# Kernel tuning notes

Hardware: AMD Instinct MI355X
Metric: run time of the kernel (lower is better)

Reference implementation:

```python
import jax, jax.numpy as jnp
import numpy as np
import math

B, L, D, H = 2, 2048, 1024, 16
DH = D // H  # 64


def setup_inputs() -> dict:
    key = jax.random.key(0)
    ks = jax.random.split(key, 8)
    s = 1.0 / math.sqrt(D)
    return {
        "query": jax.random.normal(ks[0], (B, L, D), dtype=jnp.float32),
        "key": jax.random.normal(ks[1], (B, L, D), dtype=jnp.float32),
        "value": jax.random.normal(ks[2], (B, L, D), dtype=jnp.float32),
        "attn_mask": jax.random.bernoulli(ks[3], 0.1, (B, L, L)),  # True = masked
        "Wq": jax.random.normal(ks[4], (D, D), dtype=jnp.float32) * s,
        "Wk": jax.random.normal(ks[5], (D, D), dtype=jnp.float32) * s,
        "Wv": jax.random.normal(ks[6], (D, D), dtype=jnp.float32) * s,
        "Wo": jax.random.normal(ks[7], (D, D), dtype=jnp.float32) * s,
    }


def reference(query, key, value, attn_mask, Wq, Wk, Wv, Wo):
    # torch nn.Linear computes x @ W.T (bias=False here)
    def shape(x):
        b, l, _ = x.shape
        return x.reshape(b, l, H, DH).transpose(0, 2, 1, 3)  # [B,H,L,DH]

    q = shape(query @ Wq.T) / jnp.sqrt(jnp.float32(DH))
    k = shape(key @ Wk.T)
    v = shape(value @ Wv.T)

    scores = jnp.einsum("bhqd,bhkd->bhqk", q, k)  # [B,H,Q,K]
    if attn_mask is not None:
        scores = jnp.where(attn_mask[:, None, :, :], jnp.float32(-1e18), scores)
    attn = jax.nn.softmax(scores, axis=-1)
    # dropout p=0.0 (eval/deterministic) -> identity
    context = jnp.einsum("bhqk,bhkd->bhqd", attn, v)
    context = context.transpose(0, 2, 1, 3).reshape(query.shape[0], -1, D)
    output = context @ Wo.T
    top_attn = attn[:, 0, :, :]
    return output, top_attn
```

## Files before the change

kernel.cpp:

```cpp
#include <hip/hip_runtime.h>

#define BB 2
#define LL 2048
#define DD 1024
#define HH 16
#define DHH 64

typedef _Float16 f16;
typedef _Float16 f16x8 __attribute__((ext_vector_type(8)));
typedef _Float16 f16x4 __attribute__((ext_vector_type(4)));
typedef _Float16 f16x2 __attribute__((ext_vector_type(2)));
typedef float f32x4 __attribute__((ext_vector_type(4)));
typedef unsigned long long u64;

#define VWAIT(N) asm volatile("s_waitcnt vmcnt(" #N ")" ::: "memory")
#define SB0() __builtin_amdgcn_sched_barrier(0)

__device__ __forceinline__ void gload_lds16(const void* g, void* l) {
    __builtin_amdgcn_global_load_lds(
        (const __attribute__((address_space(1))) void*)g,
        (__attribute__((address_space(3))) void*)l, 16, 0, 0);
}

__device__ __forceinline__ f16x4 cvt4f(float4 v) {
    f16x4 o;
    o[0] = (f16)v.x; o[1] = (f16)v.y; o[2] = (f16)v.z; o[3] = (f16)v.w;
    return o;
}

__global__ void prep(const float* __restrict__ q, const float* __restrict__ k,
                     const float* __restrict__ v, const int* __restrict__ msk,
                     const float* __restrict__ wq, const float* __restrict__ wk,
                     const float* __restrict__ wv, const float* __restrict__ wo,
                     f16* __restrict__ bufQ, f16* __restrict__ bufK, f16* __restrict__ bufV,
                     f16* __restrict__ wh, u64* __restrict__ Mp, float scq) {
    const int tid = threadIdx.x;
    const int y = blockIdx.y;
    if (y == 0) {
        const int lane = tid & 63;
        int w = (blockIdx.x * 256 + tid) >> 6;
        const int nw = (1024 * 256) >> 6;
        for (; w < BB * LL * 32; w += nw) {
            int mv = msk[(size_t)w * 64 + lane];
            u64 bits = __ballot(mv != 0);
            if (lane == 0) {
                const int kt = w & 31;
                const int bq = w >> 5;
                const int qq = bq & 2047, b = bq >> 11;
                Mp[((size_t)b * 32 + kt) * LL + qq] = bits;
            }
        }
    } else if (y == 1) {
        int i = blockIdx.x * 256 + tid;
        const int stride = 1024 * 256;
        for (; i < 4 * 262144; i += stride) {
            const int sel = i >> 18, j = i & 262143;
            const float* s = sel == 0 ? wq : sel == 1 ? wk : sel == 2 ? wv : wo;
            ((f16x4*)wh)[i] = cvt4f(((const float4*)s)[j]);
        }
    } else {
        const float* s = y == 2 ? q : y == 3 ? k : v;
        f16* o = y == 2 ? bufQ : y == 3 ? bufK : bufV;
        const float sc = y == 2 ? scq : 1.0f;
        int i = blockIdx.x * 256 + tid;
        const int stride = 1024 * 256;
        for (; i < (int)(BB * LL * DD / 4); i += stride) {
            float4 vv = ((const float4*)s)[i];
            vv.x *= sc; vv.y *= sc; vv.z *= sc; vv.w *= sc;
            ((f16x4*)o)[i] = cvt4f(vv);
        }
    }
}

__global__ void cvt_kernel(const float* __restrict__ src, f16* __restrict__ dst, int n4, float sc) {
    int i = blockIdx.x * blockDim.x + threadIdx.x;
    const int stride = gridDim.x * blockDim.x;
    for (; i < n4; i += stride) {
        float4 v = ((const float4*)src)[i];
        v.x *= sc; v.y *= sc; v.z *= sc; v.w *= sc;
        ((f16x4*)dst)[i] = cvt4f(v);
    }
}
__global__ void cvt4_kernel(const float* __restrict__ a, const float* __restrict__ b,
                            const float* __restrict__ c, const float* __restrict__ d,
                            f16* __restrict__ dst, int n4) {
    const float* s = blockIdx.y == 0 ? a : blockIdx.y == 1 ? b : blockIdx.y == 2 ? c : d;
    f16* o = dst + (size_t)blockIdx.y * n4 * 4;
    int i = blockIdx.x * blockDim.x + threadIdx.x;
    const int stride = gridDim.x * blockDim.x;
    for (; i < n4; i += stride)
        ((f16x4*)o)[i] = cvt4f(((const float4*)s)[i]);
}
__global__ void pack_mask(const int* __restrict__ mask, u64* __restrict__ out, int nwords) {
    const int lane = threadIdx.x & 63;
    int w = (blockIdx.x * blockDim.x + threadIdx.x) >> 6;
    const int nw = (gridDim.x * blockDim.x) >> 6;
    for (; w < nwords; w += nw) {
        int mv = mask[(size_t)w * 64 + lane];
        u64 bits = __ballot(mv != 0);
        if (lane == 0) {
            const int kt = w & 31;
            const int bq = w >> 5;
            const int qq = bq & 2047, b = bq >> 11;
            out[((size_t)b * 32 + kt) * LL + qq] = bits;
        }
    }
}

__device__ __forceinline__ void gemm_core(const f16* __restrict__ A, const f16* __restrict__ W,
                                          f16* __restrict__ C, int z, int xb, int yb, char* lds) {
    const int tid = threadIdx.x, wid = tid >> 6, lane = tid & 63;
    const int m0 = yb * 128, n0 = xb * 128;
    const int lq = lane & 15, lg = lane >> 4;
    const int wm = (wid >> 1) << 6, wn = (wid & 1) << 6;
    f32x4 acc[4][4] = {};

    #pragma unroll
    for (int t = 0; t < 2; ++t)
        #pragma unroll
        for (int j = 0; j < 2; ++j) {
            const int ldsoff = (wid * 2 + j) << 10;
            const int o = ldsoff + lane * 16;
            const int row = o >> 6, c8 = (o >> 4) & 3;
            gload_lds16(A + (size_t)(m0 + row) * DD + t * 32 + c8 * 8, lds + t * 8192 + ldsoff);
            gload_lds16(W + (size_t)(n0 + row) * DD + t * 32 + c8 * 8, lds + 24576 + t * 8192 + ldsoff);
        }

    for (int kt = 0; kt < 32; ++kt) {
        VWAIT(4);
        SB0();
        __builtin_amdgcn_s_barrier();
        SB0();
        {
            const int nk = (kt + 2 < 32) ? kt + 2 : 31;
            const int nb = (kt + 2) % 3;
            #pragma unroll
            for (int j = 0; j < 2; ++j) {
                const int ldsoff = (wid * 2 + j) << 10;
                const int o = ldsoff + lane * 16;
                const int row = o >> 6, c8 = (o >> 4) & 3;
                gload_lds16(A + (size_t)(m0 + row) * DD + nk * 32 + c8 * 8,
                            lds + nb * 8192 + ldsoff);
                gload_lds16(W + (size_t)(n0 + row) * DD + nk * 32 + c8 * 8,
                            lds + 24576 + nb * 8192 + ldsoff);
            }
        }
        SB0();

        const int cb = kt % 3;
        const char* Ab = lds + cb * 8192;
        const char* Bb = lds + 24576 + cb * 8192;
        f16x8 af[4], bf[4];
        #pragma unroll
        for (int m = 0; m < 4; ++m)
            af[m] = *(const f16x8*)(Ab + (wm + m * 16 + lq) * 64 + lg * 16);
        #pragma unroll
        for (int n = 0; n < 4; ++n)
            bf[n] = *(const f16x8*)(Bb + (wn + n * 16 + lq) * 64 + lg * 16);
        __builtin_amdgcn_s_setprio(1);
        #pragma unroll
        for (int m = 0; m < 4; ++m)
            #pragma unroll
            for (int n = 0; n < 4; ++n)
                acc[m][n] = __builtin_amdgcn_mfma_f32_16x16x32_f16(af[m], bf[n], acc[m][n], 0, 0, 0);
        __builtin_amdgcn_s_setprio(0);
    }

    #pragma unroll
    for (int m = 0; m < 4; ++m)
        #pragma unroll
        for (int n = 0; n < 4; ++n)
            #pragma unroll
            for (int r = 0; r < 4; ++r) {
                const int row = m0 + wm + m * 16 + lg * 4 + r;
                const int col = n0 + wn + n * 16 + lq;
                const float val = acc[m][n][r];
                if (z < 2) {
                    C[(size_t)row * DD + col] = (f16)val;
                } else {
                    const int b = row >> 11, l = row & 2047;
                    const int h = col >> 6, dh = col & 63;
                    C[((size_t)((b * HH + h) * DHH + dh) << 11) + l] = (f16)val;
                }
            }
}

__global__ __launch_bounds__(256) void gemm_qkv(
        const f16* __restrict__ A0, const f16* __restrict__ A1, const f16* __restrict__ A2,
        const f16* __restrict__ W0, const f16* __restrict__ W1, const f16* __restrict__ W2,
        f16* __restrict__ C0, f16* __restrict__ C1, f16* __restrict__ C2) {
    __shared__ __align__(16) char lds[49152];
    const int bid = blockIdx.x;
    const int xcd = bid & 7, j = bid >> 3;
    const int p = xcd * 12 + (j >> 3);
    const int xb = j & 7;
    const int z = p >> 5, yb = p & 31;
    const f16* A = z == 0 ? A0 : z == 1 ? A1 : A2;
    const f16* W = z == 0 ? W0 : z == 1 ? W1 : W2;
    f16* C       = z == 0 ? C0 : z == 1 ? C1 : C2;
    gemm_core(A, W, C, z, xb, yb, lds);
}

__global__ __launch_bounds__(256) void gemm_one(const f16* __restrict__ A, const f16* __restrict__ W,
                                                f16* __restrict__ C, int z) {
    __shared__ __align__(16) char lds[49152];
    gemm_core(A, W, C, z, blockIdx.x, blockIdx.y, lds);
}

template<bool TOPF16>
__global__ __launch_bounds__(256) void finale(const f16* __restrict__ A, const f16* __restrict__ W,
                                              float* __restrict__ C, float* __restrict__ top,
                                              const void* __restrict__ src,
                                              const float* __restrict__ linvp) {
    __shared__ __align__(16) char lds[36864];
    const int tid = threadIdx.x;
    if (blockIdx.x >= 512) {
        int i = (blockIdx.x - 512) * 256 + tid;
        const int stride = 1024 * 256;
        if (TOPF16) {
            const f16x8* s8 = (const f16x8*)src;
            const int n = (int)((size_t)BB * LL * LL / 8);
            for (; i < n; i += stride) {
                f16x8 v = s8[i];
                const float linv = linvp[(i * 8) >> 11];
                float4 a, bq;
                a.x = (float)v[0] * linv; a.y = (float)v[1] * linv;
                a.z = (float)v[2] * linv; a.w = (float)v[3] * linv;
                bq.x = (float)v[4] * linv; bq.y = (float)v[5] * linv;
                bq.z = (float)v[6] * linv; bq.w = (float)v[7] * linv;
                ((float4*)top)[i * 2] = a;
                ((float4*)top)[i * 2 + 1] = bq;
            }
        } else {
            const int n = (int)((size_t)BB * LL * LL / 4);
            for (; i < n; i += stride) {
                float4 v = ((const float4*)top)[i];
                const float linv = linvp[(i * 4) >> 11];
                v.x = __builtin_amdgcn_exp2f(v.x) * linv;
                v.y = __builtin_amdgcn_exp2f(v.y) * linv;
                v.z = __builtin_amdgcn_exp2f(v.z) * linv;
                v.w = __builtin_amdgcn_exp2f(v.w) * linv;
                ((float4*)top)[i] = v;
            }
        }
        return;
    }
    const int bid = blockIdx.x;
    const int xcd = bid & 7, j = bid >> 3;
    const int yb = xcd * 4 + (j >> 4);
    const int xb = j & 15;
    const int wid = tid >> 6, lane = tid & 63;
    const int m0 = yb * 128, n0 = xb * 64;
    const int lq = lane & 15, lg = lane >> 4;
    const int wm = wid * 32;
    f32x4 acc[2][4] = {};

    #pragma unroll
    for (int t = 0; t < 2; ++t) {
        #pragma unroll
        for (int j2 = 0; j2 < 2; ++j2) {
            const int o = (j2 * 256 + tid) * 16;
            const int row = o >> 6, c8 = (o >> 4) & 3;
            gload_lds16(A + (size_t)(m0 + row) * DD + t * 32 + c8 * 8,
                        lds + t * 8192 + j2 * 4096 + (wid << 10));
        }
        {
            const int o = tid * 16;
            const int row = o >> 6, c8 = (o >> 4) & 3;
            gload_lds16(W + (size_t)(n0 + row) * DD + t * 32 + c8 * 8,
                        lds + 24576 + t * 4096 + (wid << 10));
        }
    }

    for (int kt = 0; kt < 32; ++kt) {
        VWAIT(3);
        SB0();
        __builtin_amdgcn_s_barrier();
        SB0();
        {
            const int nk = (kt + 2 < 32) ? kt + 2 : 31;
            const int nb = (kt + 2) % 3;
            #pragma unroll
            for (int j2 = 0; j2 < 2; ++j2) {
                const int o = (j2 * 256 + tid) * 16;
                const int row = o >> 6, c8 = (o >> 4) & 3;
                gload_lds16(A + (size_t)(m0 + row) * DD + nk * 32 + c8 * 8,
                            lds + nb * 8192 + j2 * 4096 + (wid << 10));
            }
            {
                const int o = tid * 16;
                const int row = o >> 6, c8 = (o >> 4) & 3;
                gload_lds16(W + (size_t)(n0 + row) * DD + nk * 32 + c8 * 8,
                            lds + 24576 + nb * 4096 + (wid << 10));
            }
        }
        SB0();

        const int cb = kt % 3;
        const char* Ab = lds + cb * 8192;
        const char* Bb = lds + 24576 + cb * 4096;
        f16x8 af[2], bf[4];
        #pragma unroll
        for (int m = 0; m < 2; ++m)
            af[m] = *(const f16x8*)(Ab + (wm + m * 16 + lq) * 64 + lg * 16);
        #pragma unroll
        for (int n = 0; n < 4; ++n)
            bf[n] = *(const f16x8*)(Bb + (n * 16 + lq) * 64 + lg * 16);
        __builtin_amdgcn_s_setprio(1);
        #pragma unroll
        for (int m = 0; m < 2; ++m)
            #pragma unroll
            for (int n = 0; n < 4; ++n)
                acc[m][n] = __builtin_amdgcn_mfma_f32_16x16x32_f16(af[m], bf[n], acc[m][n], 0, 0, 0);
        __builtin_amdgcn_s_setprio(0);
    }

    #pragma unroll
    for (int m = 0; m < 2; ++m)
        #pragma unroll
        for (int n = 0; n < 4; ++n)
            #pragma unroll
            for (int r = 0; r < 4; ++r) {
                const int row = m0 + wm + m * 16 + lg * 4 + r;
                const int col = n0 + n * 16 + lq;
                C[(size_t)row * DD + col] = acc[m][n][r];
            }
}

template<bool TOPF16>
__global__ __launch_bounds__(512) void attn_fwd(const f16* __restrict__ Qp, const f16* __restrict__ Kp,
                                                const f16* __restrict__ VTp,
                                                const u64* __restrict__ Mp,
                                                f16* __restrict__ Op, void* __restrict__ topout,
                                                float* __restrict__ statsLinv) {
    extern __shared__ char lds[];
    const int tid = threadIdx.x, wid = tid >> 6, lane = tid & 63;
    const int lq = lane & 15, lg = lane >> 4;
    const int bid = blockIdx.x;
    const int xcd = bid & 7, j = bid >> 3;
    const int bh = xcd * 4 + (j >> 4);
    const int qt = j & 15;
    const int b = bh >> 4, h = bh & 15;
    const bool topblk = (h == 0);
    const int qrow = qt * 128 + wid * 16 + lq;

    const int srow = tid >> 3;
    const int ssc = ((tid & 7) ^ (srow & 7));
    const f16* ksrc = Kp + (size_t)(b * LL + srow) * DD + h * 64 + ssc * 8;
    const f16* vsrc = VTp + (size_t)((b * HH + h) * DHH + srow) * LL + ssc * 8;
    char* kdst = lds + 16384 + (wid << 10);
    char* vdst = lds + 49152 + (wid << 10);

    f16x8 qf[2];
    #pragma unroll
    for (int kk = 0; kk < 2; ++kk)
        qf[kk] = *(const f16x8*)(Qp + (size_t)(b * LL + qrow) * DD + h * 64 + (kk * 4 + lg) * 8);

    #pragma unroll
    for (int t = 0; t < 2; ++t) {
        gload_lds16(ksrc + (size_t)t * 64 * DD, kdst + t * 8192);
        gload_lds16(vsrc + t * 64, vdst + t * 8192);
    }

    float lsum = 0.f;
    f32x4 acc[4] = {};

    for (int it = 0; it < 16; ++it) {
        const int kt0 = it * 2;
        if (topblk && it > 0) { VWAIT(8); } else { VWAIT(0); }
        SB0();
        __builtin_amdgcn_s_barrier();
        SB0();
        const u64 cm0 = Mp[((size_t)b * 32 + kt0) * LL + qrow];
        const u64 cm1 = Mp[((size_t)b * 32 + kt0 + 1) * LL + qrow];
        SB0();
        #pragma unroll
        for (int t = 0; t < 2; ++t) {
            const int nk = (kt0 + 2 + t < 32) ? kt0 + 2 + t : 31;
            const int nb = (kt0 + 2 + t) & 3;
            gload_lds16(ksrc + (size_t)nk * 64 * DD, kdst + nb * 8192);
            gload_lds16(vsrc + nk * 64, vdst + nb * 8192);
        }
        SB0();

        #pragma unroll
        for (int t = 0; t < 2; ++t) {
            const int cb = (kt0 + t) & 3;
            const char* Kb = lds + 16384 + cb * 8192;
            const char* Vb = lds + 49152 + cb * 8192;
            const u64 cm = t == 0 ? cm0 : cm1;

            f32x4 s[4] = {};
            __builtin_amdgcn_s_setprio(1);
            #pragma unroll
            for (int f = 0; f < 4; ++f)
                #pragma unroll
                for (int kk = 0; kk < 2; ++kk) {
                    const int co = (((kk * 4 + lg) ^ (lq & 7)) << 4);
                    f16x8 kf = *(const f16x8*)(Kb + (f * 16 + lq) * 128 + co);
                    s[f] = __builtin_amdgcn_mfma_f32_16x16x32_f16(kf, qf[kk], s[f], 0, 0, 0);
                }
            __builtin_amdgcn_s_setprio(0);

            const u64 wsh = cm >> (lg * 4);
            const unsigned lo = (unsigned)wsh, hi = (unsigned)(wsh >> 32);
            f16x4 ph[4];
            #pragma unroll
            for (int f = 0; f < 4; ++f) {
                const unsigned nib = ((f < 2) ? (lo >> (f * 16)) : (hi >> ((f - 2) * 16))) & 0xFu;
                #pragma unroll
                for (int r = 0; r < 4; ++r)
                    if (nib & (1u << r)) s[f][r] = -1e18f;
                const float p0 = __builtin_amdgcn_exp2f(s[f][0]);
                const float p1 = __builtin_amdgcn_exp2f(s[f][1]);
                const float p2 = __builtin_amdgcn_exp2f(s[f][2]);
                const float p3 = __builtin_amdgcn_exp2f(s[f][3]);
                lsum += (p0 + p1) + (p2 + p3);
                f16x2 pa = __builtin_bit_cast(f16x2, __builtin_amdgcn_cvt_pkrtz(p0, p1));
                f16x2 pb = __builtin_bit_cast(f16x2, __builtin_amdgcn_cvt_pkrtz(p2, p3));
                ph[f][0] = pa[0]; ph[f][1] = pa[1]; ph[f][2] = pb[0]; ph[f][3] = pb[1];
            }

            if (topblk) {
                if (TOPF16) {
                    f16* T = (f16*)topout;
                    #pragma unroll
                    for (int f = 0; f < 4; ++f)
                        *(f16x4*)(T + ((size_t)b * LL + qrow) * LL + (kt0 + t) * 64 + f * 16 + lg * 4) = ph[f];
                } else {
                    float* T = (float*)topout;
                    #pragma unroll
                    for (int f = 0; f < 4; ++f)
                        *(f32x4*)(T + ((size_t)b * LL + qrow) * LL + (kt0 + t) * 64 + f * 16 + lg * 4) = s[f];
                }
            }

            #pragma unroll
            for (int f = 0; f < 4; ++f) {
                const int chunk = f * 2 + (lg >> 1);
                const int bo = ((chunk ^ (lq & 7)) << 4) + (lg & 1) * 8;
                *(f16x4*)(lds + (wid << 11) + lq * 128 + bo) = ph[f];
            }

            __builtin_amdgcn_s_setprio(1);
            #pragma unroll
            for (int kk = 0; kk < 2; ++kk) {
                const int co = (((kk * 4 + lg) ^ (lq & 7)) << 4);
                f16x8 pf = *(const f16x8*)(lds + (wid << 11) + lq * 128 + co);
                #pragma unroll
                for (int f = 0; f < 4; ++f) {
                    f16x8 vf = *(const f16x8*)(Vb + (f * 16 + lq) * 128 + co);
                    acc[f] = __builtin_amdgcn_mfma_f32_16x16x32_f16(vf, pf, acc[f], 0, 0, 0);
                }
            }
            __builtin_amdgcn_s_setprio(0);
        }
    }

    lsum += __shfl_xor(lsum, 16);
    lsum += __shfl_xor(lsum, 32);
    const float linv = 1.f / lsum;
    #pragma unroll
    for (int f = 0; f < 4; ++f) {
        f16x4 ov;
        #pragma unroll
        for (int r = 0; r < 4; ++r) ov[r] = (f16)(acc[f][r] * linv);
        *(f16x4*)(Op + (size_t)(b * LL + qrow) * DD + h * 64 + f * 16 + lg * 4) = ov;
    }
    if (topblk && lg == 0) statsLinv[(size_t)b * LL + qrow] = linv;
}

extern "C" void kernel_launch(void* const* d_in, const int* in_sizes, int n_in,
                              void* d_out, int out_size, void* d_ws, size_t ws_size,
                              hipStream_t stream) {
    const float* q   = (const float*)d_in[0];
    const float* k   = (const float*)d_in[1];
    const float* v   = (const float*)d_in[2];
    const int*   msk = (const int*)d_in[3];
    const float* wq  = (const float*)d_in[4];
    const float* wk  = (const float*)d_in[5];
    const float* wv  = (const float*)d_in[6];
    const float* wo  = (const float*)d_in[7];
    float* out = (float*)d_out;

    const size_t NX = (size_t)BB * LL * DD;
    const size_t NW = (size_t)DD * DD;
    const int NMW = BB * LL * (LL / 64);
    const size_t NXo = NX;
    const float SCQ = 0.125f * 1.4426950408889634f;
    const int ALDS = 81920;

    hipFuncSetAttribute(reinterpret_cast<const void*>(attn_fwd<true>),
                        hipFuncAttributeMaxDynamicSharedMemorySize, ALDS);
    hipFuncSetAttribute(reinterpret_cast<const void*>(attn_fwd<false>),
                        hipFuncAttributeMaxDynamicSharedMemorySize, ALDS);

    f16* ws = (f16*)d_ws;
    const size_t needed = (6 * NX + 4 * NW) * 2 + (size_t)NMW * 8 + (size_t)BB * LL * 4;
    const bool fused = ws_size >= needed;

    if (fused) {
        f16* bufQ = ws;
        f16* bufK = bufQ + NX;
        f16* bufV = bufK + NX;
        f16* Op   = bufQ;
        f16* topP = bufK;
        f16* wh   = bufV + NX;
        f16* wqh = wh, *wkh = wh + NW, *wvh = wh + 2 * NW, *woh = wh + 3 * NW;
        f16* Qp  = wh + 4 * NW;
        f16* Kp  = Qp + NX;
        f16* VTp = Kp + NX;
        u64* Mp  = (u64*)(VTp + NX);
        float* statsLinv = (float*)(Mp + NMW);

        prep<<<dim3(1024, 5), 256, 0, stream>>>(q, k, v, msk, wq, wk, wv, wo,
                                                bufQ, bufK, bufV, wh, Mp, SCQ);
        gemm_qkv<<<768, 256, 0, stream>>>(bufQ, bufK, bufV, wqh, wkh, wvh, Qp, Kp, VTp);
        attn_fwd<true><<<512, 512, ALDS, stream>>>(Qp, Kp, VTp, Mp, Op, topP, statsLinv);
        finale<true><<<1536, 256, 0, stream>>>(Op, woh, out, out + NXo, topP, statsLinv);
    } else {
        f16* bufA = ws;
        f16* wh   = bufA + NX;
        f16* wqh = wh, *wkh = wh + NW, *wvh = wh + 2 * NW, *woh = wh + 3 * NW;
        f16* Qp  = wh + 4 * NW;
        f16* Kp  = Qp + NX;
        f16* VTp = Kp + NX;
        u64* Mp  = (u64*)(VTp + NX);
        float* statsLinv = (float*)(Mp + NMW);

        pack_mask<<<256, 256, 0, stream>>>(msk, Mp, NMW);
        cvt4_kernel<<<dim3(128, 4), 256, 0, stream>>>(wq, wk, wv, wo, wh, (int)(NW / 4));
        cvt_kernel<<<2048, 256, 0, stream>>>(q, bufA, (int)(NX / 4), SCQ);
        gemm_one<<<dim3(8, 32), 256, 0, stream>>>(bufA, wqh, Qp, 0);
        cvt_kernel<<<2048, 256, 0, stream>>>(k, bufA, (int)(NX / 4), 1.f);
        gemm_one<<<dim3(8, 32), 256, 0, stream>>>(bufA, wkh, Kp, 1);
        cvt_kernel<<<2048, 256, 0, stream>>>(v, bufA, (int)(NX / 4), 1.f);
        gemm_one<<<dim3(8, 32), 256, 0, stream>>>(bufA, wvh, VTp, 2);
        attn_fwd<false><<<512, 512, ALDS, stream>>>(Qp, Kp, VTp, Mp, bufA,
                                                    out + NXo, statsLinv);
        finale<false><<<1536, 256, 0, stream>>>(bufA, woh, out, out + NXo, out + NXo, statsLinv);
    }
}
```

Baseline: 159.9 us.

## Move mask packing into QKV GEMM launch and prefetch mask words in attention

Mask bit-packing moves out of the prep kernel and into 128 extra blocks of the QKV GEMM launch, so it runs alongside the projection GEMMs instead of lengthening prep. In the attention kernel, the per-iteration mask word loads are software-pipelined one iteration ahead using ping-pong registers through a manually unrolled lambda, which hides their global-load latency. The costs are extra registers, mask blocks competing with GEMM blocks for CUs, and a changed block-to-XCD mapping in the GEMM.

```diff
diff --git a/kernel.cpp b/kernel.cpp
--- a/kernel.cpp
+++ b/kernel.cpp
@@ -29,28 +29,14 @@
 }
 
 __global__ void prep(const float* __restrict__ q, const float* __restrict__ k,
-                     const float* __restrict__ v, const int* __restrict__ msk,
+                     const float* __restrict__ v,
                      const float* __restrict__ wq, const float* __restrict__ wk,
                      const float* __restrict__ wv, const float* __restrict__ wo,
                      f16* __restrict__ bufQ, f16* __restrict__ bufK, f16* __restrict__ bufV,
-                     f16* __restrict__ wh, u64* __restrict__ Mp, float scq) {
+                     f16* __restrict__ wh, float scq) {
     const int tid = threadIdx.x;
     const int y = blockIdx.y;
     if (y == 0) {
-        const int lane = tid & 63;
-        int w = (blockIdx.x * 256 + tid) >> 6;
-        const int nw = (1024 * 256) >> 6;
-        for (; w < BB * LL * 32; w += nw) {
-            int mv = msk[(size_t)w * 64 + lane];
-            u64 bits = __ballot(mv != 0);
-            if (lane == 0) {
-                const int kt = w & 31;
-                const int bq = w >> 5;
-                const int qq = bq & 2047, b = bq >> 11;
-                Mp[((size_t)b * 32 + kt) * LL + qq] = bits;
-            }
-        }
-    } else if (y == 1) {
         int i = blockIdx.x * 256 + tid;
         const int stride = 1024 * 256;
         for (; i < 4 * 262144; i += stride) {
@@ -59,9 +45,9 @@
             ((f16x4*)wh)[i] = cvt4f(((const float4*)s)[j]);
         }
     } else {
-        const float* s = y == 2 ? q : y == 3 ? k : v;
-        f16* o = y == 2 ? bufQ : y == 3 ? bufK : bufV;
-        const float sc = y == 2 ? scq : 1.0f;
+        const float* s = y == 1 ? q : y == 2 ? k : v;
+        f16* o = y == 1 ? bufQ : y == 2 ? bufK : bufV;
+        const float sc = y == 1 ? scq : 1.0f;
         int i = blockIdx.x * 256 + tid;
         const int stride = 1024 * 256;
         for (; i < (int)(BB * LL * DD / 4); i += stride) {
@@ -188,9 +174,27 @@
 __global__ __launch_bounds__(256) void gemm_qkv(
         const f16* __restrict__ A0, const f16* __restrict__ A1, const f16* __restrict__ A2,
         const f16* __restrict__ W0, const f16* __restrict__ W1, const f16* __restrict__ W2,
-        f16* __restrict__ C0, f16* __restrict__ C1, f16* __restrict__ C2) {
+        f16* __restrict__ C0, f16* __restrict__ C1, f16* __restrict__ C2,
+        const int* __restrict__ msk, u64* __restrict__ Mp) {
     __shared__ __align__(16) char lds[49152];
-    const int bid = blockIdx.x;
+    const int tid = threadIdx.x;
+    if (blockIdx.x < 128) {
+        const int lane = tid & 63;
+        int w = (blockIdx.x * 256 + tid) >> 6;
+        const int nw = (128 * 256) >> 6;
+        for (; w < BB * LL * 32; w += nw) {
+            int mv = msk[(size_t)w * 64 + lane];
+            u64 bits = __ballot(mv != 0);
+            if (lane == 0) {
+                const int kt = w & 31;
+                const int bq = w >> 5;
+                const int qq = bq & 2047, b = bq >> 11;
+                Mp[((size_t)b * 32 + kt) * LL + qq] = bits;
+            }
+        }
+        return;
+    }
+    const int bid = blockIdx.x - 128;
     const int xcd = bid & 7, j = bid >> 3;
     const int p = xcd * 12 + (j >> 3);
     const int xb = j & 7;
@@ -350,12 +354,16 @@
     const f16* vsrc = VTp + (size_t)((b * HH + h) * DHH + srow) * LL + ssc * 8;
     char* kdst = lds + 16384 + (wid << 10);
     char* vdst = lds + 49152 + (wid << 10);
+    const u64* mrow = Mp + (size_t)b * 32 * LL + qrow;
 
     f16x8 qf[2];
     #pragma unroll
     for (int kk = 0; kk < 2; ++kk)
         qf[kk] = *(const f16x8*)(Qp + (size_t)(b * LL + qrow) * DD + h * 64 + (kk * 4 + lg) * 8);
 
+    u64 cmA0 = mrow[0 * LL], cmA1 = mrow[1 * LL];
+    u64 cmB0 = 0, cmB1 = 0;
+    SB0();
     #pragma unroll
     for (int t = 0; t < 2; ++t) {
         gload_lds16(ksrc + (size_t)t * 64 * DD, kdst + t * 8192);
@@ -365,14 +373,17 @@
     float lsum = 0.f;
     f32x4 acc[4] = {};
 
-    for (int it = 0; it < 16; ++it) {
-        const int kt0 = it * 2;
-        if (topblk && it > 0) { VWAIT(8); } else { VWAIT(0); }
+    auto body = [&](int kt0, u64 cmU0, u64 cmU1, u64& cmL0, u64& cmL1) {
+        if (topblk && kt0 > 0) { VWAIT(8); } else { VWAIT(0); }
         SB0();
         __builtin_amdgcn_s_barrier();
         SB0();
-        const u64 cm0 = Mp[((size_t)b * 32 + kt0) * LL + qrow];
-        const u64 cm1 = Mp[((size_t)b * 32 + kt0 + 1) * LL + qrow];
+        {
+            const int n0k = (kt0 + 2 < 32) ? kt0 + 2 : 31;
+            const int n1k = (kt0 + 3 < 32) ? kt0 + 3 : 31;
+            cmL0 = mrow[(size_t)n0k * LL];
+            cmL1 = mrow[(size_t)n1k * LL];
+        }
         SB0();
         #pragma unroll
         for (int t = 0; t < 2; ++t) {
@@ -388,7 +399,7 @@
             const int cb = (kt0 + t) & 3;
             const char* Kb = lds + 16384 + cb * 8192;
             const char* Vb = lds + 49152 + cb * 8192;
-            const u64 cm = t == 0 ? cm0 : cm1;
+            const u64 cm = t == 0 ? cmU0 : cmU1;
 
             f32x4 s[4] = {};
             __builtin_amdgcn_s_setprio(1);
@@ -455,6 +466,11 @@
             }
             __builtin_amdgcn_s_setprio(0);
         }
+    };
+
+    for (int k2 = 0; k2 < 8; ++k2) {
+        body(k2 * 4,     cmA0, cmA1, cmB0, cmB1);
+        body(k2 * 4 + 2, cmB0, cmB1, cmA0, cmA1);
     }
 
     lsum += __shfl_xor(lsum, 16);
@@ -513,9 +529,10 @@
         u64* Mp  = (u64*)(VTp + NX);
         float* statsLinv = (float*)(Mp + NMW);
 
-        prep<<<dim3(1024, 5), 256, 0, stream>>>(q, k, v, msk, wq, wk, wv, wo,
-                                                bufQ, bufK, bufV, wh, Mp, SCQ);
-        gemm_qkv<<<768, 256, 0, stream>>>(bufQ, bufK, bufV, wqh, wkh, wvh, Qp, Kp, VTp);
+        prep<<<dim3(1024, 4), 256, 0, stream>>>(q, k, v, wq, wk, wv, wo,
+                                                bufQ, bufK, bufV, wh, SCQ);
+        gemm_qkv<<<896, 256, 0, stream>>>(bufQ, bufK, bufV, wqh, wkh, wvh, Qp, Kp, VTp,
+                                          msk, Mp);
         attn_fwd<true><<<512, 512, ALDS, stream>>>(Qp, Kp, VTp, Mp, Op, topP, statsLinv);
         finale<true><<<1536, 256, 0, stream>>>(Op, woh, out, out + NXo, topP, statsLinv);
     } else {
```

Result: slower. 214.9 us (+34.4%).
